# Kernel optimization log

Measured on AMD Instinct MI355X. Metric: run time of the kernel, lower is better.

The kernel has to match this reference:

```python
import jax, jax.numpy as jnp
import numpy as np

D_MODEL = 1024
N_HEAD = 16
SEQ = 1024
BATCH = 4
D_K = D_MODEL // N_HEAD
LN_EPS = 1e-6


def setup_inputs() -> dict:
    key = jax.random.key(0)
    ks = jax.random.split(key, 10)
    scale = 1.0 / np.sqrt(D_MODEL)
    return {
        "q": jax.random.normal(ks[0], (SEQ, BATCH, D_MODEL), jnp.float32),
        "k": jax.random.normal(ks[1], (SEQ, BATCH, D_MODEL), jnp.float32),
        "v": jax.random.normal(ks[2], (SEQ, BATCH, D_MODEL), jnp.float32),
        "sph": jax.random.uniform(ks[3], (BATCH, N_HEAD, SEQ, SEQ), jnp.float32),
        "Wq": jax.random.normal(ks[4], (D_MODEL, D_MODEL), jnp.float32) * scale,
        "Wk": jax.random.normal(ks[5], (D_MODEL, D_MODEL), jnp.float32) * scale,
        "Wv": jax.random.normal(ks[6], (D_MODEL, D_MODEL), jnp.float32) * scale,
        "Wo": jax.random.normal(ks[7], (D_MODEL, D_MODEL), jnp.float32) * scale,
        "gamma": jnp.ones((D_MODEL,), jnp.float32),
        "beta": jnp.zeros((D_MODEL,), jnp.float32),
    }


def reference(q, k, v, sph, Wq, Wk, Wv, Wo, gamma, beta):
    # q,k,v: [S, B, D] -> batch-first [B, S, D]
    qb = jnp.swapaxes(q, 0, 1)
    kb = jnp.swapaxes(k, 0, 1)
    vb = jnp.swapaxes(v, 0, 1)
    B, S, D = qb.shape
    residual = qb
    # projections (nn.Linear: y = x @ W.T), split heads -> [B, H, S, d_k]
    qh = (qb @ Wq.T).reshape(B, S, N_HEAD, D_K).transpose(0, 2, 1, 3)
    kh = (kb @ Wk.T).reshape(B, S, N_HEAD, D_K).transpose(0, 2, 1, 3)
    vh = (vb @ Wv.T).reshape(B, S, N_HEAD, D_K).transpose(0, 2, 1, 3)
    temp = jnp.float32(np.sqrt(D_K))
    # attention logits with spatial modulation
    attn = jnp.einsum("bhqd,bhkd->bhqk", qh / temp, kh) * sph
    p_attn = jax.nn.softmax(attn, axis=-1)  # dropout = identity (eval)
    out = jnp.einsum("bhqk,bhkd->bhqd", p_attn, vh)
    out = out.transpose(0, 2, 1, 3).reshape(B, S, D)
    out = out @ Wo.T + residual
    # LayerNorm over last dim, eps=1e-6
    mu = jnp.mean(out, axis=-1, keepdims=True)
    var = jnp.var(out, axis=-1, keepdims=True)
    out = (out - mu) * jax.lax.rsqrt(var + LN_EPS) * gamma + beta
    return jnp.swapaxes(out, 0, 1), p_attn
```

## Files before the change

### kernel.cpp

```cpp
#include <hip/hip_runtime.h>
#include <hip/hip_bf16.h>
#include <hip/hip_fp16.h>
#include <cstdint>

constexpr int B_ = 4, H_ = 16, S_ = 1024, D_ = 1024, DK_ = 64;

typedef __bf16 bf16x8 __attribute__((ext_vector_type(8)));
typedef float f32x4 __attribute__((ext_vector_type(4)));
#define MFMA16(a, b, c) __builtin_amdgcn_mfma_f32_16x16x32_bf16(a, b, c, 0, 0, 0)

static __device__ inline unsigned short f2bf(float f) {
  __hip_bfloat16 h = __float2bfloat16(f);
  return *reinterpret_cast<unsigned short*>(&h);
}
static __device__ inline unsigned packbf(float lo, float hi) {
  return ((unsigned)f2bf(hi) << 16) | (unsigned)f2bf(lo);
}
static __device__ inline unsigned pack_f16(float x, float y) {
  __half hx = __float2half(x), hy = __float2half(y);
  return ((unsigned)(*reinterpret_cast<unsigned short*>(&hy)) << 16) |
         (unsigned)(*reinterpret_cast<unsigned short*>(&hx));
}
static __device__ inline float f16lo(unsigned u) {
  unsigned short s = (unsigned short)(u & 0xffff);
  return __half2float(*reinterpret_cast<__half*>(&s));
}
static __device__ inline float f16hi(unsigned u) {
  unsigned short s = (unsigned short)(u >> 16);
  return __half2float(*reinterpret_cast<__half*>(&s));
}

__global__ __launch_bounds__(256) void k_cvt3(const float* __restrict__ x0,
                                              const float* __restrict__ x1,
                                              const float* __restrict__ x2,
                                              __hip_bfloat16* __restrict__ y0,
                                              __hip_bfloat16* __restrict__ y1,
                                              __hip_bfloat16* __restrict__ y2) {
  const int sel = blockIdx.x >> 12;
  const int i = (blockIdx.x & 4095) * 256 + threadIdx.x;
  const float* x = sel == 0 ? x0 : (sel == 1 ? x1 : x2);
  __hip_bfloat16* y = sel == 0 ? y0 : (sel == 1 ? y1 : y2);
  const float4 v = reinterpret_cast<const float4*>(x)[i];
  ushort4 o;
  o.x = f2bf(v.x); o.y = f2bf(v.y); o.z = f2bf(v.z); o.w = f2bf(v.w);
  *reinterpret_cast<ushort4*>(&y[(size_t)i * 4]) = o;
}

__global__ __launch_bounds__(256) void k_cvt4(const float* __restrict__ x0,
                                              const float* __restrict__ x1,
                                              const float* __restrict__ x2,
                                              const float* __restrict__ x3,
                                              __hip_bfloat16* __restrict__ y0,
                                              __hip_bfloat16* __restrict__ y1,
                                              __hip_bfloat16* __restrict__ y2,
                                              __hip_bfloat16* __restrict__ y3) {
  const int sel = blockIdx.x >> 10;
  const int i = (blockIdx.x & 1023) * 256 + threadIdx.x;
  const float* x = sel == 0 ? x0 : (sel == 1 ? x1 : (sel == 2 ? x2 : x3));
  __hip_bfloat16* y = sel == 0 ? y0 : (sel == 1 ? y1 : (sel == 2 ? y2 : y3));
  const float4 v = reinterpret_cast<const float4*>(x)[i];
  ushort4 o;
  o.x = f2bf(v.x); o.y = f2bf(v.y); o.z = f2bf(v.z); o.w = f2bf(v.w);
  *reinterpret_cast<ushort4*>(&y[(size_t)i * 4]) = o;
}

template <int MODE>
__global__ __launch_bounds__(256) void k_gemm(const __hip_bfloat16* __restrict__ A,
                                              const __hip_bfloat16* __restrict__ Bw,
                                              const float* __restrict__ resid,
                                              __hip_bfloat16* __restrict__ Yb,
                                              float* __restrict__ Yf) {
  __shared__ __hip_bfloat16 Als[128 * 64];
  __shared__ __hip_bfloat16 Bls[64 * 64];
  const int tid = threadIdx.x;
  const int lane = tid & 63;
  const int l15 = lane & 15, g = lane >> 4;
  const int w = tid >> 6;
  const int wr = w >> 1, wc = w & 1;
  const int rt = blockIdx.x, ct = blockIdx.y;
  f32x4 acc[4][2] = {};

  for (int k0 = 0; k0 < D_; k0 += 64) {
#pragma unroll
    for (int q = 0; q < 4; ++q) {
      const int slot0 = q * 256 + (tid & 192);
      const int slot = slot0 + lane;
      const int r = slot >> 3, p = slot & 7;
      const int lc = p ^ (r & 7);
      const __hip_bfloat16* src = A + (size_t)(rt * 128 + r) * D_ + k0 + lc * 8;
      __builtin_amdgcn_global_load_lds(
          (const __attribute__((address_space(1))) unsigned int*)src,
          (__attribute__((address_space(3))) unsigned int*)&Als[slot0 * 8], 16, 0, 0);
    }
#pragma unroll
    for (int q = 0; q < 2; ++q) {
      const int slot0 = q * 256 + (tid & 192);
      const int slot = slot0 + lane;
      const int r = slot >> 3, p = slot & 7;
      const int lc = p ^ (r & 7);
      const __hip_bfloat16* src = Bw + (size_t)(ct * 64 + r) * D_ + k0 + lc * 8;
      __builtin_amdgcn_global_load_lds(
          (const __attribute__((address_space(1))) unsigned int*)src,
          (__attribute__((address_space(3))) unsigned int*)&Bls[slot0 * 8], 16, 0, 0);
    }
    __syncthreads();
#pragma unroll
    for (int ks = 0; ks < 2; ++ks) {
      bf16x8 bfr[2];
#pragma unroll
      for (int cf = 0; cf < 2; ++cf) {
        const int r = wc * 32 + cf * 16 + l15;
        const int p = (ks * 4 + g) ^ (r & 7);
        bfr[cf] = *reinterpret_cast<const bf16x8*>(&Bls[(r * 8 + p) * 8]);
      }
#pragma unroll
      for (int fi = 0; fi < 4; ++fi) {
        const int r = wr * 64 + fi * 16 + l15;
        const int p = (ks * 4 + g) ^ (r & 7);
        const bf16x8 af = *reinterpret_cast<const bf16x8*>(&Als[(r * 8 + p) * 8]);
        acc[fi][0] = MFMA16(af, bfr[0], acc[fi][0]);
        acc[fi][1] = MFMA16(af, bfr[1], acc[fi][1]);
      }
    }
    __syncthreads();
  }
#pragma unroll
  for (int fi = 0; fi < 4; ++fi)
#pragma unroll
    for (int cf = 0; cf < 2; ++cf)
#pragma unroll
      for (int r = 0; r < 4; ++r) {
        const int m = rt * 128 + wr * 64 + fi * 16 + 4 * g + r;
        const int t = wc * 32 + cf * 16 + l15;
        const float val = acc[fi][cf][r];
        if (MODE == 0) {
          const int s = m >> 2, b = m & 3;
          Yb[((size_t)((b * H_ + ct) * S_ + s)) * DK_ + t] = __float2bfloat16(val);
        } else if (MODE == 1) {
          const int s = m >> 2, b = m & 3;
          Yb[((size_t)((b * H_ + ct) * DK_ + t)) * S_ + s] = __float2bfloat16(val);
        } else {
          const int b = m >> 10, s = m & 1023;
          const int o = ct * 64 + t;
          Yf[(size_t)m * D_ + o] = val + resid[(size_t)(s * B_ + b) * D_ + o];
        }
      }
}

__global__ __launch_bounds__(256, 4) void k_attn(const __hip_bfloat16* __restrict__ Qh,
                                                 const __hip_bfloat16* __restrict__ Kh,
                                                 const __hip_bfloat16* __restrict__ VT,
                                                 const float* __restrict__ sph,
                                                 float* __restrict__ Pout,
                                                 __hip_bfloat16* __restrict__ O) {
  __shared__ unsigned int Plds[16 * 512];
  const int tid = threadIdx.x, lane = tid & 63, w = tid >> 6;
  const int l15 = lane & 15, g = lane >> 4;
  const int it = blockIdx.x, bh = blockIdx.y;
  const unsigned sw = (unsigned)((l15 & 7) << 2);

  {
    const __hip_bfloat16* qp = Qh + ((size_t)bh * S_ + it * 16 + l15) * DK_ + 8 * g;
    const bf16x8 qf0 = *reinterpret_cast<const bf16x8*>(qp);
    const bf16x8 qf1 = *reinterpret_cast<const bf16x8*>(qp + 32);
    const __hip_bfloat16* kb0 =
        Kh + (size_t)bh * S_ * DK_ + (size_t)(w * 256 + l15) * DK_ + 8 * g;
    bf16x8 kra[2], krb[2], krc[2], krd[2];
    kra[0] = *reinterpret_cast<const bf16x8*>(kb0);
    krb[0] = *reinterpret_cast<const bf16x8*>(kb0 + 32);
    krc[0] = *reinterpret_cast<const bf16x8*>(kb0 + 16 * DK_);
    krd[0] = *reinterpret_cast<const bf16x8*>(kb0 + 16 * DK_ + 32);
#pragma unroll
    for (int j = 0; j < 8; ++j) {
      const int cur = j & 1, nxt = cur ^ 1;
      if (j < 7) {
        const __hip_bfloat16* kp = kb0 + (size_t)(j + 1) * 32 * DK_;
        kra[nxt] = *reinterpret_cast<const bf16x8*>(kp);
        krb[nxt] = *reinterpret_cast<const bf16x8*>(kp + 32);
        krc[nxt] = *reinterpret_cast<const bf16x8*>(kp + 16 * DK_);
        krd[nxt] = *reinterpret_cast<const bf16x8*>(kp + 16 * DK_ + 32);
      }
      f32x4 a0 = {0.f, 0.f, 0.f, 0.f};
      f32x4 a1 = {0.f, 0.f, 0.f, 0.f};
      __builtin_amdgcn_s_setprio(1);
      a0 = MFMA16(kra[cur], qf0, a0);
      a0 = MFMA16(krb[cur], qf1, a0);
      a1 = MFMA16(krc[cur], qf0, a1);
      a1 = MFMA16(krd[cur], qf1, a1);
      __builtin_amdgcn_s_setprio(0);
      const int key0 = w * 256 + j * 32;
      uint2 u0, u1;
      u0.x = pack_f16(a0[0] * 0.125f, a0[1] * 0.125f);
      u0.y = pack_f16(a0[2] * 0.125f, a0[3] * 0.125f);
      u1.x = pack_f16(a1[0] * 0.125f, a1[1] * 0.125f);
      u1.y = pack_f16(a1[2] * 0.125f, a1[3] * 0.125f);
      const int base0 = l15 * 512 + (key0 >> 1) + 2 * g;
      *reinterpret_cast<uint2*>(&Plds[(unsigned)base0 ^ sw]) = u0;
      *reinterpret_cast<uint2*>(&Plds[(unsigned)(base0 + 8) ^ sw]) = u1;
    }
  }
  __syncthreads();

  {
    const float4* sbase = reinterpret_cast<const float4*>(
        sph + ((size_t)bh << 20) + (((size_t)(it * 16)) << 10));
    float4 svbuf[2][4];
#pragma unroll
    for (int i = 0; i < 4; ++i)
      svbuf[0][i] = sbase[(size_t)(w * 4) * 256 + lane + 64 * i];
#pragma unroll
    for (int rr = 0; rr < 4; ++rr) {
      const int row = w * 4 + rr;
      if (rr < 3) {
#pragma unroll
        for (int i = 0; i < 4; ++i)
          svbuf[(rr + 1) & 1][i] = sbase[(size_t)(row + 1) * 256 + lane + 64 * i];
      }
      const unsigned rsw = (unsigned)((row & 7) << 2);
      const int lbase = row * 512;
      uint2 uv[4];
#pragma unroll
      for (int i = 0; i < 4; ++i)
        uv[i] = *reinterpret_cast<uint2*>(
            &Plds[(unsigned)(lbase + 2 * lane + 128 * i) ^ rsw]);
      float va[16];
#pragma unroll
      for (int i = 0; i < 4; ++i) {
        const float4 sv = svbuf[rr & 1][i];
        va[4 * i + 0] = f16lo(uv[i].x) * sv.x;
        va[4 * i + 1] = f16hi(uv[i].x) * sv.y;
        va[4 * i + 2] = f16lo(uv[i].y) * sv.z;
        va[4 * i + 3] = f16hi(uv[i].y) * sv.w;
      }
      float m = va[0];
#pragma unroll
      for (int i = 1; i < 16; ++i) m = fmaxf(m, va[i]);
#pragma unroll
      for (int off = 1; off < 64; off <<= 1) m = fmaxf(m, __shfl_xor(m, off));
      float sum = 0.f;
#pragma unroll
      for (int i = 0; i < 16; ++i) {
        va[i] = __expf(va[i] - m);
        sum += va[i];
      }
#pragma unroll
      for (int off = 1; off < 64; off <<= 1) sum += __shfl_xor(sum, off);
      const float inv = 1.f / sum;
      float4* po = reinterpret_cast<float4*>(Pout + ((size_t)bh << 20) +
                                             (((size_t)(it * 16 + row)) << 10));
#pragma unroll
      for (int i = 0; i < 4; ++i) {
        float4 p;
        p.x = va[4 * i + 0] * inv;
        p.y = va[4 * i + 1] * inv;
        p.z = va[4 * i + 2] * inv;
        p.w = va[4 * i + 3] * inv;
        po[lane + 64 * i] = p;
        uint2 pb;
        pb.x = packbf(p.x, p.y);
        pb.y = packbf(p.z, p.w);
        *reinterpret_cast<uint2*>(
            &Plds[(unsigned)(lbase + 2 * lane + 128 * i) ^ rsw]) = pb;
      }
    }
  }
  __syncthreads();

  {
    const int c0 = w * 16;
    f32x4 o0 = {0.f, 0.f, 0.f, 0.f};
    const __hip_bfloat16* vb =
        VT + (size_t)bh * DK_ * S_ + (size_t)(c0 + l15) * S_ + 8 * g;
#pragma unroll
    for (int kb2 = 0; kb2 < 4; ++kb2) {
      bf16x8 vreg[8];
      bf16x8 preg[8];
#pragma unroll
      for (int u = 0; u < 8; ++u)
        vreg[u] = *reinterpret_cast<const bf16x8*>(vb + kb2 * 256 + u * 32);
#pragma unroll
      for (int u = 0; u < 8; ++u) {
        const int k0 = kb2 * 256 + u * 32;
        preg[u] = *reinterpret_cast<const bf16x8*>(
            &Plds[(unsigned)(l15 * 512 + (k0 >> 1) + 4 * g) ^ sw]);
      }
      __builtin_amdgcn_s_setprio(1);
#pragma unroll
      for (int u = 0; u < 8; ++u) o0 = MFMA16(preg[u], vreg[u], o0);
      __builtin_amdgcn_s_setprio(0);
    }
    const int b = bh >> 4, h = bh & 15;
#pragma unroll
    for (int r = 0; r < 4; ++r) {
      const int srow = it * 16 + 4 * g + r;
      O[((size_t)(b * S_ + srow)) * D_ + h * DK_ + c0 + l15] = __float2bfloat16(o0[r]);
    }
  }
}

__global__ __launch_bounds__(256) void k_ln(const float* __restrict__ Z,
                                            const float* __restrict__ gamma,
                                            const float* __restrict__ beta,
                                            float* __restrict__ out) {
  const int r = blockIdx.x;
  const int b = r >> 10, s = r & 1023;
  const int tid = threadIdx.x;
  const float4 z = *reinterpret_cast<const float4*>(Z + (size_t)r * D_ + (tid << 2));
  float sum = z.x + z.y + z.z + z.w;
  float sq = z.x * z.x + z.y * z.y + z.z * z.z + z.w * z.w;
#pragma unroll
  for (int off = 1; off < 64; off <<= 1) {
    sum += __shfl_xor(sum, off);
    sq += __shfl_xor(sq, off);
  }
  __shared__ float rs[4];
  __shared__ float rq[4];
  const int wv = tid >> 6, ln = tid & 63;
  if (ln == 0) { rs[wv] = sum; rq[wv] = sq; }
  __syncthreads();
  const float tsum = rs[0] + rs[1] + rs[2] + rs[3];
  const float tsq = rq[0] + rq[1] + rq[2] + rq[3];
  const float mu = tsum * (1.0f / 1024.0f);
  const float var = tsq * (1.0f / 1024.0f) - mu * mu;
  const float rstd = rsqrtf(var + 1e-6f);
  const float4 gm = *reinterpret_cast<const float4*>(gamma + (tid << 2));
  const float4 bt = *reinterpret_cast<const float4*>(beta + (tid << 2));
  float4 o;
  o.x = (z.x - mu) * rstd * gm.x + bt.x;
  o.y = (z.y - mu) * rstd * gm.y + bt.y;
  o.z = (z.z - mu) * rstd * gm.z + bt.z;
  o.w = (z.w - mu) * rstd * gm.w + bt.w;
  *reinterpret_cast<float4*>(out + (size_t)(s * B_ + b) * D_ + (tid << 2)) = o;
}

extern "C" void kernel_launch(void* const* d_in, const int* in_sizes, int n_in,
                              void* d_out, int out_size, void* d_ws, size_t ws_size,
                              hipStream_t stream) {
  const float* q = (const float*)d_in[0];
  const float* k = (const float*)d_in[1];
  const float* v = (const float*)d_in[2];
  const float* sph = (const float*)d_in[3];
  const float* Wq = (const float*)d_in[4];
  const float* Wk = (const float*)d_in[5];
  const float* Wv = (const float*)d_in[6];
  const float* Wo = (const float*)d_in[7];
  const float* gamma = (const float*)d_in[8];
  const float* beta = (const float*)d_in[9];

  float* out = (float*)d_out;
  float* P = out + (size_t)4 * 1024 * 1024;

  char* ws = (char*)d_ws;
  __hip_bfloat16* xq = (__hip_bfloat16*)(ws);
  __hip_bfloat16* xk = (__hip_bfloat16*)(ws + ((size_t)8 << 20));
  __hip_bfloat16* xv = (__hip_bfloat16*)(ws + ((size_t)16 << 20));
  __hip_bfloat16* wqb = (__hip_bfloat16*)(ws + ((size_t)24 << 20));
  __hip_bfloat16* wkb = (__hip_bfloat16*)(ws + ((size_t)26 << 20));
  __hip_bfloat16* wvb = (__hip_bfloat16*)(ws + ((size_t)28 << 20));
  __hip_bfloat16* wob = (__hip_bfloat16*)(ws + ((size_t)30 << 20));
  __hip_bfloat16* Qh = (__hip_bfloat16*)(ws + ((size_t)32 << 20));
  __hip_bfloat16* Khb = (__hip_bfloat16*)(ws + ((size_t)40 << 20));
  __hip_bfloat16* VTb = (__hip_bfloat16*)(ws + ((size_t)48 << 20));
  __hip_bfloat16* Ob = (__hip_bfloat16*)(ws + ((size_t)56 << 20));
  float* Z = (float*)(ws + ((size_t)64 << 20));

  const dim3 blk(256);
  k_cvt3<<<12288, blk, 0, stream>>>(q, k, v, xq, xk, xv);
  k_cvt4<<<4096, blk, 0, stream>>>(Wq, Wk, Wv, Wo, wqb, wkb, wvb, wob);

  k_gemm<0><<<dim3(32, 16), blk, 0, stream>>>(xq, wqb, nullptr, Qh, nullptr);
  k_gemm<0><<<dim3(32, 16), blk, 0, stream>>>(xk, wkb, nullptr, Khb, nullptr);
  k_gemm<1><<<dim3(32, 16), blk, 0, stream>>>(xv, wvb, nullptr, VTb, nullptr);

  k_attn<<<dim3(64, 64), blk, 0, stream>>>(Qh, Khb, VTb, sph, P, Ob);

  k_gemm<2><<<dim3(32, 16), blk, 0, stream>>>(Ob, wob, q, nullptr, Z);
  k_ln<<<4096, blk, 0, stream>>>(Z, gamma, beta, out);
}
```

Measured before the change: 286.2 us.

## Stream sph rows into LDS via global_load_lds and use exp2 softmax

Loads of the sph modulation rows now go through direct global-to-LDS transfers (global_load_lds) into a per-wave LDS buffer instead of register-prefetched float4 loads. The first row is issued before QK^T so its fetch overlaps the MFMA phase, and each next row is issued during the current row's softmax. The logit scale folds in log2(e) so exp2f replaces __expf. This adds 16KB of LDS per block, which may lower occupancy. The s_waitcnt vmcnt(0) also waits on outstanding Pout stores, which could serialize the row loop.

```diff
diff --git a/kernel.cpp b/kernel.cpp
--- a/kernel.cpp
+++ b/kernel.cpp
@@ -154,10 +154,25 @@
                                                  float* __restrict__ Pout,
                                                  __hip_bfloat16* __restrict__ O) {
   __shared__ unsigned int Plds[16 * 512];
+  __shared__ float sphl[4][1024];
   const int tid = threadIdx.x, lane = tid & 63, w = tid >> 6;
   const int l15 = lane & 15, g = lane >> 4;
   const int it = blockIdx.x, bh = blockIdx.y;
   const unsigned sw = (unsigned)((l15 & 7) << 2);
+  const int wrow = w * 4;
+  constexpr float kScale = 0.125f * 1.44269504088896f;
+
+  auto dma_row = [&](int rr) {
+    const float* src = sph + ((size_t)bh << 20) +
+                       (((size_t)(it * 16 + wrow + rr)) << 10) + lane * 4;
+#pragma unroll
+    for (int i = 0; i < 4; ++i)
+      __builtin_amdgcn_global_load_lds(
+          (const __attribute__((address_space(1))) unsigned int*)(src + i * 256),
+          (__attribute__((address_space(3))) unsigned int*)&sphl[w][i * 256], 16, 0, 0);
+  };
+
+  dma_row(0);
 
   {
     const __hip_bfloat16* qp = Qh + ((size_t)bh * S_ + it * 16 + l15) * DK_ + 8 * g;
@@ -190,10 +205,10 @@
       __builtin_amdgcn_s_setprio(0);
       const int key0 = w * 256 + j * 32;
       uint2 u0, u1;
-      u0.x = pack_f16(a0[0] * 0.125f, a0[1] * 0.125f);
-      u0.y = pack_f16(a0[2] * 0.125f, a0[3] * 0.125f);
-      u1.x = pack_f16(a1[0] * 0.125f, a1[1] * 0.125f);
-      u1.y = pack_f16(a1[2] * 0.125f, a1[3] * 0.125f);
+      u0.x = pack_f16(a0[0] * kScale, a0[1] * kScale);
+      u0.y = pack_f16(a0[2] * kScale, a0[3] * kScale);
+      u1.x = pack_f16(a1[0] * kScale, a1[1] * kScale);
+      u1.y = pack_f16(a1[2] * kScale, a1[3] * kScale);
       const int base0 = l15 * 512 + (key0 >> 1) + 2 * g;
       *reinterpret_cast<uint2*>(&Plds[(unsigned)base0 ^ sw]) = u0;
       *reinterpret_cast<uint2*>(&Plds[(unsigned)(base0 + 8) ^ sw]) = u1;
@@ -201,67 +216,62 @@
   }
   __syncthreads();
 
-  {
-    const float4* sbase = reinterpret_cast<const float4*>(
-        sph + ((size_t)bh << 20) + (((size_t)(it * 16)) << 10));
-    float4 svbuf[2][4];
+#pragma unroll
+  for (int rr = 0; rr < 4; ++rr) {
+    if (rr > 0) {
+      asm volatile("s_waitcnt vmcnt(0)" ::: "memory");
+      __builtin_amdgcn_sched_barrier(0);
+    }
+    const int row = wrow + rr;
+    float4 sv[4];
 #pragma unroll
     for (int i = 0; i < 4; ++i)
-      svbuf[0][i] = sbase[(size_t)(w * 4) * 256 + lane + 64 * i];
-#pragma unroll
-    for (int rr = 0; rr < 4; ++rr) {
-      const int row = w * 4 + rr;
-      if (rr < 3) {
-#pragma unroll
-        for (int i = 0; i < 4; ++i)
-          svbuf[(rr + 1) & 1][i] = sbase[(size_t)(row + 1) * 256 + lane + 64 * i];
-      }
-      const unsigned rsw = (unsigned)((row & 7) << 2);
-      const int lbase = row * 512;
-      uint2 uv[4];
-#pragma unroll
-      for (int i = 0; i < 4; ++i)
-        uv[i] = *reinterpret_cast<uint2*>(
-            &Plds[(unsigned)(lbase + 2 * lane + 128 * i) ^ rsw]);
-      float va[16];
-#pragma unroll
-      for (int i = 0; i < 4; ++i) {
-        const float4 sv = svbuf[rr & 1][i];
-        va[4 * i + 0] = f16lo(uv[i].x) * sv.x;
-        va[4 * i + 1] = f16hi(uv[i].x) * sv.y;
-        va[4 * i + 2] = f16lo(uv[i].y) * sv.z;
-        va[4 * i + 3] = f16hi(uv[i].y) * sv.w;
-      }
-      float m = va[0];
-#pragma unroll
-      for (int i = 1; i < 16; ++i) m = fmaxf(m, va[i]);
-#pragma unroll
-      for (int off = 1; off < 64; off <<= 1) m = fmaxf(m, __shfl_xor(m, off));
-      float sum = 0.f;
-#pragma unroll
-      for (int i = 0; i < 16; ++i) {
-        va[i] = __expf(va[i] - m);
-        sum += va[i];
-      }
-#pragma unroll
-      for (int off = 1; off < 64; off <<= 1) sum += __shfl_xor(sum, off);
-      const float inv = 1.f / sum;
-      float4* po = reinterpret_cast<float4*>(Pout + ((size_t)bh << 20) +
-                                             (((size_t)(it * 16 + row)) << 10));
-#pragma unroll
-      for (int i = 0; i < 4; ++i) {
-        float4 p;
-        p.x = va[4 * i + 0] * inv;
-        p.y = va[4 * i + 1] * inv;
-        p.z = va[4 * i + 2] * inv;
-        p.w = va[4 * i + 3] * inv;
-        po[lane + 64 * i] = p;
-        uint2 pb;
-        pb.x = packbf(p.x, p.y);
-        pb.y = packbf(p.z, p.w);
-        *reinterpret_cast<uint2*>(
-            &Plds[(unsigned)(lbase + 2 * lane + 128 * i) ^ rsw]) = pb;
-      }
+      sv[i] = reinterpret_cast<const float4*>(&sphl[w][0])[lane + 64 * i];
+    const unsigned rsw = (unsigned)((row & 7) << 2);
+    const int lbase = row * 512;
+    uint2 uv[4];
+#pragma unroll
+    for (int i = 0; i < 4; ++i)
+      uv[i] = *reinterpret_cast<uint2*>(
+          &Plds[(unsigned)(lbase + 2 * lane + 128 * i) ^ rsw]);
+    float va[16];
+#pragma unroll
+    for (int i = 0; i < 4; ++i) {
+      va[4 * i + 0] = f16lo(uv[i].x) * sv[i].x;
+      va[4 * i + 1] = f16hi(uv[i].x) * sv[i].y;
+      va[4 * i + 2] = f16lo(uv[i].y) * sv[i].z;
+      va[4 * i + 3] = f16hi(uv[i].y) * sv[i].w;
+    }
+    if (rr < 3) dma_row(rr + 1);
+    float m = va[0];
+#pragma unroll
+    for (int i = 1; i < 16; ++i) m = fmaxf(m, va[i]);
+#pragma unroll
+    for (int off = 1; off < 64; off <<= 1) m = fmaxf(m, __shfl_xor(m, off));
+    float sum = 0.f;
+#pragma unroll
+    for (int i = 0; i < 16; ++i) {
+      va[i] = exp2f(va[i] - m);
+      sum += va[i];
+    }
+#pragma unroll
+    for (int off = 1; off < 64; off <<= 1) sum += __shfl_xor(sum, off);
+    const float inv = 1.f / sum;
+    float4* po = reinterpret_cast<float4*>(Pout + ((size_t)bh << 20) +
+                                           (((size_t)(it * 16 + row)) << 10));
+#pragma unroll
+    for (int i = 0; i < 4; ++i) {
+      float4 p;
+      p.x = va[4 * i + 0] * inv;
+      p.y = va[4 * i + 1] * inv;
+      p.z = va[4 * i + 2] * inv;
+      p.w = va[4 * i + 3] * inv;
+      po[lane + 64 * i] = p;
+      uint2 pb;
+      pb.x = packbf(p.x, p.y);
+      pb.y = packbf(p.z, p.w);
+      *reinterpret_cast<uint2*>(
+          &Plds[(unsigned)(lbase + 2 * lane + 128 * i) ^ rsw]) = pb;
     }
   }
   __syncthreads();
```

New measurement: 284.7 us. About the same (-0.5%).
